# Performance work log

Hardware: AMD Instinct MI355X
Metric: run time of the kernel (lower is better)

Reference implementation:

```python
import jax, jax.numpy as jnp
import numpy as np

BETA = 10.0  # fixed buffer: torch.ones(1, num_centers) * 10


def setup_inputs() -> dict:
    key = jax.random.key(0)
    k1, k2, k3 = jax.random.split(key, 3)
    n, M, d, n_out = 65536, 1024, 64, 3
    x = jax.random.normal(k1, (n, d), dtype=jnp.float32)
    centers = jax.random.normal(k2, (M, d), dtype=jnp.float32)
    # nn.Linear init in the module: weight ~ N(0, 0.02), bias = 0
    W = jax.random.normal(k3, (n_out, M + d), dtype=jnp.float32) * 0.02
    b = jnp.zeros((n_out,), dtype=jnp.float32)
    return {"x": x, "centers": centers, "W": W, "b": b}


def reference(x, centers, W, b):
    x2 = jnp.sum(x * x, axis=1, keepdims=True)          # [n, 1]
    c2 = jnp.sum(centers * centers, axis=1)             # [M]
    d2 = x2 + c2[None, :] - 2.0 * (x @ centers.T)       # [n, M]
    rbf = jnp.exp(-BETA * d2)                           # Gaussian RBF
    feat = jnp.concatenate([x, rbf], axis=1)            # [n, d + M]
    return feat @ W.T + b                               # [n, n_out]
```

## Files before the change

### kernel.cpp

```cpp
#include <hip/hip_runtime.h>
#include <math.h>

typedef short bf16x8 __attribute__((ext_vector_type(8)));
typedef float f32x4 __attribute__((ext_vector_type(4)));
typedef unsigned int uint32;

#define BETA 10.0f
#define THRESH -80.0f

#define C_OFF   0
#define XB_OFF  131072
#define RED_OFF 147456
#define LDS_TOT 150528

__device__ __forceinline__ uint32 f2bf_rtne(float f) {
    uint32 u = __float_as_uint(f);
    u += 0x7FFFu + ((u >> 16) & 1u);
    return u >> 16;
}
__device__ __forceinline__ uint32 pk_rtne(float a, float b) {
    return f2bf_rtne(a) | (f2bf_rtne(b) << 16);
}
__device__ __forceinline__ f32x4 vmax4(f32x4 a, f32x4 b) {
    f32x4 r;
    r[0] = fmaxf(a[0], b[0]); r[1] = fmaxf(a[1], b[1]);
    r[2] = fmaxf(a[2], b[2]); r[3] = fmaxf(a[3], b[3]);
    return r;
}
#define MFMA __builtin_amdgcn_mfma_f32_16x16x32_bf16

__global__ __launch_bounds__(512) void rbfn_fused(
    const float* __restrict__ x,
    const float* __restrict__ centers,
    const float* __restrict__ W,
    const float* __restrict__ bias,
    float* __restrict__ out)
{
    __shared__ __align__(16) char lds[LDS_TOT];

    const int tid = threadIdx.x;
    const int wv = tid >> 6;
    const int lane = tid & 63;
    const int quad = lane >> 4;
    const int l15 = lane & 15;
    const int row0 = blockIdx.x * 256;

    float4 x0[4], x1[4];
    {
        const float4* xg = (const float4*)(x + (size_t)row0 * 64);
        #pragma unroll
        for (int i = 0; i < 4; ++i) x0[i] = xg[i * 512 + tid];
        #pragma unroll
        for (int i = 0; i < 4; ++i) x1[i] = xg[2048 + i * 512 + tid];
    }

    {
        const float4* cf4 = (const float4*)centers;
        #pragma unroll 8
        for (int i = 0; i < 32; ++i) {
            const int f = i * 512 + tid;
            const float4 v = cf4[f];
            const int j = f >> 4, sg = f & 15;
            uint2 q; q.x = pk_rtne(v.x, v.y); q.y = pk_rtne(v.z, v.w);
            *(uint2*)(lds + C_OFF + (j >> 4) * 2048 + (sg >> 1) * 256 +
                      (j & 15) * 16 + (sg & 1) * 8) = q;
        }
    }
    #pragma unroll
    for (int i = 0; i < 4; ++i) {
        const int f = i * 512 + tid;
        const float4 v = x0[i];
        const int r = f >> 4, sg = f & 15;
        uint2 q; q.x = pk_rtne(v.x, v.y); q.y = pk_rtne(v.z, v.w);
        *(uint2*)(lds + XB_OFF + (r >> 4) * 2048 + (sg >> 1) * 256 +
                  (r & 15) * 16 + (sg & 1) * 8) = q;
    }

    bf16x8 bwh[2], bwl[2];
    float bl = 0.f;
    if (wv == 0) {
        if (l15 < 3) bl = bias[l15];
        #pragma unroll
        for (int kk = 0; kk < 2; ++kk) {
            bf16x8 h, l;
            #pragma unroll
            for (int e = 0; e < 8; ++e) {
                const float w = (l15 < 3) ? W[l15 * 1088 + kk * 32 + quad * 8 + e] : 0.f;
                const uint32 hb = f2bf_rtne(w);
                h[e] = (short)hb;
                l[e] = (short)f2bf_rtne(w - __uint_as_float(hb << 16));
            }
            bwh[kk] = h; bwl[kk] = l;
        }
    }

    __syncthreads();

    const char* cB = lds + C_OFF + wv * 16384 + quad * 256 + l15 * 16;
    float c2r[8];

    #pragma unroll
    for (int t = 0; t < 2; ++t) {
        bf16x8 af[8][2];
        #pragma unroll
        for (int rt = 0; rt < 8; ++rt) {
            const char* ab = lds + XB_OFF + rt * 2048 + l15 * 16;
            af[rt][0] = *(const bf16x8*)(ab + quad * 256);
            af[rt][1] = *(const bf16x8*)(ab + (4 + quad) * 256);
        }

        float mn = 1e30f;
        #pragma unroll
        for (int rt = 0; rt < 8; ++rt) {
            const f32x4 z = {0.f, 0.f, 0.f, 0.f};
            f32x4 d = MFMA(af[rt][0], af[rt][0], z, 0, 0, 0);
            d = MFMA(af[rt][1], af[rt][1], d, 0, 0, 0);
            #pragma unroll
            for (int reg = 0; reg < 4; ++reg)
                mn = fminf(mn, __shfl(d[reg], quad * 20 + reg));
        }
        const float prermax = -BETA * mn;

        if (t == 0) {
            #pragma unroll
            for (int ct = 0; ct < 8; ++ct) {
                const bf16x8 b0 = *(const bf16x8*)(cB + ct * 2048);
                const bf16x8 b1 = *(const bf16x8*)(cB + ct * 2048 + 1024);
                const f32x4 z = {0.f, 0.f, 0.f, 0.f};
                f32x4 d = MFMA(b0, b0, z, 0, 0, 0);
                d = MFMA(b1, b1, d, 0, 0, 0);
                const float dv = (l15 & 2) ? ((l15 & 1) ? d[3] : d[2])
                                           : ((l15 & 1) ? d[1] : d[0]);
                c2r[ct] = -BETA * __shfl(dv, (l15 >> 2) * 16 + l15);
            }
        }

        if (wv == 0) {
            float* redf = (float*)(lds + RED_OFF + t * 1536);
            #pragma unroll
            for (int rt = 0; rt < 8; ++rt) {
                const f32x4 z = {0.f, 0.f, 0.f, 0.f};
                f32x4 aw = MFMA(af[rt][0], bwh[0], z, 0, 0, 0);
                aw = MFMA(af[rt][1], bwh[1], aw, 0, 0, 0);
                aw = MFMA(af[rt][0], bwl[0], aw, 0, 0, 0);
                aw = MFMA(af[rt][1], bwl[1], aw, 0, 0, 0);
                if (l15 < 3) {
                    #pragma unroll
                    for (int reg = 0; reg < 4; ++reg)
                        redf[(rt * 16 + quad * 4 + reg) * 3 + l15] = aw[reg] + bl;
                }
            }
        }

        __syncthreads();

        if (t == 0) {
            #pragma unroll
            for (int i = 0; i < 4; ++i) {
                const int f = i * 512 + tid;
                const float4 v = x1[i];
                const int r = f >> 4, sg = f & 15;
                uint2 q; q.x = pk_rtne(v.x, v.y); q.y = pk_rtne(v.z, v.w);
                *(uint2*)(lds + XB_OFF + (r >> 4) * 2048 + (sg >> 1) * 256 +
                          (r & 15) * 16 + (sg & 1) * 8) = q;
            }
        }

        float gm = -1e30f;
        #pragma unroll
        for (int ct = 0; ct < 8; ++ct) {
            const bf16x8 b0 = *(const bf16x8*)(cB + ct * 2048);
            const bf16x8 b1 = *(const bf16x8*)(cB + ct * 2048 + 1024);
            f32x4 acc[8];
            #pragma unroll
            for (int rt = 0; rt < 8; ++rt) {
                const f32x4 z = {0.f, 0.f, 0.f, 0.f};
                acc[rt] = MFMA(af[rt][0], b0, z, 0, 0, 0);
                acc[rt] = MFMA(af[rt][1], b1, acc[rt], 0, 0, 0);
            }
            f32x4 m0 = vmax4(vmax4(acc[0], acc[1]), vmax4(acc[2], acc[3]));
            f32x4 m1 = vmax4(vmax4(acc[4], acc[5]), vmax4(acc[6], acc[7]));
            m0 = vmax4(m0, m1);
            const float m = fmaxf(fmaxf(m0[0], m0[1]), fmaxf(m0[2], m0[3]));
            gm = fmaxf(gm, fmaf(2.0f * BETA, m, c2r[ct]));
        }
        const float bound = gm + prermax;

        if (__builtin_expect(__ballot(bound > THRESH) != 0ull, 0)) {
            float* red = (float*)(lds + RED_OFF + t * 1536);
            #pragma clang loop unroll(disable)
            for (int ct = 0; ct < 8; ++ct) {
                const int j = wv * 128 + ct * 16 + l15;
                #pragma clang loop unroll(disable)
                for (int rr = 0; rr < 32; ++rr) {
                    const int r = (rr >> 2) * 16 + quad * 4 + (rr & 3);
                    const float* xr = x + (size_t)(row0 + t * 128 + r) * 64;
                    const float* cr = centers + (size_t)j * 64;
                    float d2 = 0.f;
                    #pragma clang loop unroll(disable)
                    for (int k = 0; k < 64; ++k) {
                        const float df = xr[k] - cr[k];
                        d2 = fmaf(df, df, d2);
                    }
                    const float arg = -BETA * d2;
                    if (arg > -87.f) {
                        const float e = expf(arg);
                        atomicAdd(&red[r * 3 + 0], e * W[0 * 1088 + 64 + j]);
                        atomicAdd(&red[r * 3 + 1], e * W[1 * 1088 + 64 + j]);
                        atomicAdd(&red[r * 3 + 2], e * W[2 * 1088 + 64 + j]);
                    }
                }
            }
        }
        __syncthreads();

        if (tid < 96)
            ((float4*)out)[blockIdx.x * 192 + t * 96 + tid] =
                *((const float4*)(lds + RED_OFF + t * 1536) + tid);
    }
}

extern "C" void kernel_launch(void* const* d_in, const int* in_sizes, int n_in,
                              void* d_out, int out_size, void* d_ws, size_t ws_size,
                              hipStream_t stream) {
    const float* x       = (const float*)d_in[0];
    const float* centers = (const float*)d_in[1];
    const float* W       = (const float*)d_in[2];
    const float* b       = (const float*)d_in[3];
    float* out = (float*)d_out;

    const int n = in_sizes[0] / 64;
    rbfn_fused<<<n / 256, 512, 0, stream>>>(x, centers, W, b, out);
}
```

Before: 81.51 us.

## Drop LDS staging, load operands into registers, halve rows per block

Result: slower. 99.60 us (+22.2%).

```diff
diff --git a/kernel.cpp b/kernel.cpp
--- a/kernel.cpp
+++ b/kernel.cpp
@@ -7,11 +7,6 @@
 
 #define BETA 10.0f
 #define THRESH -80.0f
-
-#define C_OFF   0
-#define XB_OFF  131072
-#define RED_OFF 147456
-#define LDS_TOT 150528
 
 __device__ __forceinline__ uint32 f2bf_rtne(float f) {
     uint32 u = __float_as_uint(f);
@@ -29,57 +24,81 @@
 }
 #define MFMA __builtin_amdgcn_mfma_f32_16x16x32_bf16
 
-__global__ __launch_bounds__(512) void rbfn_fused(
+__global__ __launch_bounds__(512, 2) void rbfn_fused(
     const float* __restrict__ x,
     const float* __restrict__ centers,
     const float* __restrict__ W,
     const float* __restrict__ bias,
     float* __restrict__ out)
 {
-    __shared__ __align__(16) char lds[LDS_TOT];
+    __shared__ __align__(16) float red[384];
 
     const int tid = threadIdx.x;
     const int wv = tid >> 6;
     const int lane = tid & 63;
     const int quad = lane >> 4;
     const int l15 = lane & 15;
-    const int row0 = blockIdx.x * 256;
+    const int row0 = blockIdx.x * 128;
+    const f32x4 z = {0.f, 0.f, 0.f, 0.f};
 
-    float4 x0[4], x1[4];
-    {
-        const float4* xg = (const float4*)(x + (size_t)row0 * 64);
+    bf16x8 bf[8][2];
+    #pragma unroll
+    for (int ct = 0; ct < 8; ++ct) {
+        const float* cp = centers + (size_t)(wv * 128 + ct * 16 + l15) * 64 + quad * 8;
         #pragma unroll
-        for (int i = 0; i < 4; ++i) x0[i] = xg[i * 512 + tid];
-        #pragma unroll
-        for (int i = 0; i < 4; ++i) x1[i] = xg[2048 + i * 512 + tid];
+        for (int kk = 0; kk < 2; ++kk) {
+            const float4 u0 = *(const float4*)(cp + kk * 32);
+            const float4 u1 = *(const float4*)(cp + kk * 32 + 4);
+            union { bf16x8 v; uint4 u; } t;
+            t.u.x = pk_rtne(u0.x, u0.y);
+            t.u.y = pk_rtne(u0.z, u0.w);
+            t.u.z = pk_rtne(u1.x, u1.y);
+            t.u.w = pk_rtne(u1.z, u1.w);
+            bf[ct][kk] = t.v;
+        }
     }
 
-    {
-        const float4* cf4 = (const float4*)centers;
-        #pragma unroll 8
-        for (int i = 0; i < 32; ++i) {
-            const int f = i * 512 + tid;
-            const float4 v = cf4[f];
-            const int j = f >> 4, sg = f & 15;
-            uint2 q; q.x = pk_rtne(v.x, v.y); q.y = pk_rtne(v.z, v.w);
-            *(uint2*)(lds + C_OFF + (j >> 4) * 2048 + (sg >> 1) * 256 +
-                      (j & 15) * 16 + (sg & 1) * 8) = q;
+    bf16x8 af[8][2];
+    #pragma unroll
+    for (int rt = 0; rt < 8; ++rt) {
+        const float* xp = x + (size_t)(row0 + rt * 16 + l15) * 64 + quad * 8;
+        #pragma unroll
+        for (int kk = 0; kk < 2; ++kk) {
+            const float4 u0 = *(const float4*)(xp + kk * 32);
+            const float4 u1 = *(const float4*)(xp + kk * 32 + 4);
+            union { bf16x8 v; uint4 u; } t;
+            t.u.x = pk_rtne(u0.x, u0.y);
+            t.u.y = pk_rtne(u0.z, u0.w);
+            t.u.z = pk_rtne(u1.x, u1.y);
+            t.u.w = pk_rtne(u1.z, u1.w);
+            af[rt][kk] = t.v;
         }
     }
+
+    float c2r[8];
     #pragma unroll
-    for (int i = 0; i < 4; ++i) {
-        const int f = i * 512 + tid;
-        const float4 v = x0[i];
-        const int r = f >> 4, sg = f & 15;
-        uint2 q; q.x = pk_rtne(v.x, v.y); q.y = pk_rtne(v.z, v.w);
-        *(uint2*)(lds + XB_OFF + (r >> 4) * 2048 + (sg >> 1) * 256 +
-                  (r & 15) * 16 + (sg & 1) * 8) = q;
+    for (int ct = 0; ct < 8; ++ct) {
+        f32x4 d = MFMA(bf[ct][0], bf[ct][0], z, 0, 0, 0);
+        d = MFMA(bf[ct][1], bf[ct][1], d, 0, 0, 0);
+        const float dv = (l15 & 2) ? ((l15 & 1) ? d[3] : d[2])
+                                   : ((l15 & 1) ? d[1] : d[0]);
+        c2r[ct] = -BETA * __shfl(dv, (l15 >> 2) * 16 + l15);
     }
 
-    bf16x8 bwh[2], bwl[2];
-    float bl = 0.f;
+    float mn = 1e30f;
+    #pragma unroll
+    for (int rt = 0; rt < 8; ++rt) {
+        f32x4 d = MFMA(af[rt][0], af[rt][0], z, 0, 0, 0);
+        d = MFMA(af[rt][1], af[rt][1], d, 0, 0, 0);
+        #pragma unroll
+        for (int reg = 0; reg < 4; ++reg)
+            mn = fminf(mn, __shfl(d[reg], quad * 20 + reg));
+    }
+    const float prermax = -BETA * mn;
+
     if (wv == 0) {
-        if (l15 < 3) bl = bias[l15];
+        const float bl = (l15 < 3) ? bias[l15] : 0.f;
+        bf16x8 bwh[2], bwl[2];
         #pragma unroll
         for (int kk = 0; kk < 2; ++kk) {
             bf16x8 h, l;
@@ -92,132 +111,66 @@
             }
             bwh[kk] = h; bwl[kk] = l;
         }
+        #pragma unroll
+        for (int rt = 0; rt < 8; ++rt) {
+            f32x4 aw = MFMA(af[rt][0], bwh[0], z, 0, 0, 0);
+            aw = MFMA(af[rt][1], bwh[1], aw, 0, 0, 0);
+            aw = MFMA(af[rt][0], bwl[0], aw, 0, 0, 0);
+            aw = MFMA(af[rt][1], bwl[1], aw, 0, 0, 0);
+            if (l15 < 3) {
+                #pragma unroll
+                for (int reg = 0; reg < 4; ++reg)
+                    red[(rt * 16 + quad * 4 + reg) * 3 + l15] = aw[reg] + bl;
+            }
+        }
     }
 
-    __syncthreads();
-
-    const char* cB = lds + C_OFF + wv * 16384 + quad * 256 + l15 * 16;
-    float c2r[8];
-
+    float gm = -1e30f;
     #pragma unroll
-    for (int t = 0; t < 2; ++t) {
-        bf16x8 af[8][2];
+    for (int ct = 0; ct < 8; ++ct) {
+        f32x4 acc[8];
         #pragma unroll
         for (int rt = 0; rt < 8; ++rt) {
-            const char* ab = lds + XB_OFF + rt * 2048 + l15 * 16;
-            af[rt][0] = *(const bf16x8*)(ab + quad * 256);
-            af[rt][1] = *(const bf16x8*)(ab + (4 + quad) * 256);
+            acc[rt] = MFMA(af[rt][0], bf[ct][0], z, 0, 0, 0);
+            acc[rt] = MFMA(af[rt][1], bf[ct][1], acc[rt], 0, 0, 0);
         }
+        f32x4 m0 = vmax4(vmax4(acc[0], acc[1]), vmax4(acc[2], acc[3]));
+        f32x4 m1 = vmax4(vmax4(acc[4], acc[5]), vmax4(acc[6], acc[7]));
+        m0 = vmax4(m0, m1);
+        const float m = fmaxf(fmaxf(m0[0], m0[1]), fmaxf(m0[2], m0[3]));
+        gm = fmaxf(gm, fmaf(2.0f * BETA, m, c2r[ct]));
+    }
+    const float bound = gm + prermax;
 
-        float mn = 1e30f;
-        #pragma unroll
-        for (int rt = 0; rt < 8; ++rt) {
-            const f32x4 z = {0.f, 0.f, 0.f, 0.f};
-            f32x4 d = MFMA(af[rt][0], af[rt][0], z, 0, 0, 0);
-            d = MFMA(af[rt][1], af[rt][1], d, 0, 0, 0);
-            #pragma unroll
-            for (int reg = 0; reg < 4; ++reg)
-                mn = fminf(mn, __shfl(d[reg], quad * 20 + reg));
-        }
-        const float prermax = -BETA * mn;
-
-        if (t == 0) {
-            #pragma unroll
-            for (int ct = 0; ct < 8; ++ct) {
-                const bf16x8 b0 = *(const bf16x8*)(cB + ct * 2048);
-                const bf16x8 b1 = *(const bf16x8*)(cB + ct * 2048 + 1024);
-                const f32x4 z = {0.f, 0.f, 0.f, 0.f};
-                f32x4 d = MFMA(b0, b0, z, 0, 0, 0);
-                d = MFMA(b1, b1, d, 0, 0, 0);
-                const float dv = (l15 & 2) ? ((l15 & 1) ? d[3] : d[2])
-                                           : ((l15 & 1) ? d[1] : d[0]);
-                c2r[ct] = -BETA * __shfl(dv, (l15 >> 2) * 16 + l15);
-            }
-        }
-
-        if (wv == 0) {
-            float* redf = (float*)(lds + RED_OFF + t * 1536);
-            #pragma unroll
-            for (int rt = 0; rt < 8; ++rt) {
-                const f32x4 z = {0.f, 0.f, 0.f, 0.f};
-                f32x4 aw = MFMA(af[rt][0], bwh[0], z, 0, 0, 0);
-                aw = MFMA(af[rt][1], bwh[1], aw, 0, 0, 0);
-                aw = MFMA(af[rt][0], bwl[0], aw, 0, 0, 0);
-                aw = MFMA(af[rt][1], bwl[1], aw, 0, 0, 0);
-                if (l15 < 3) {
-                    #pragma unroll
-                    for (int reg = 0; reg < 4; ++reg)
-                        redf[(rt * 16 + quad * 4 + reg) * 3 + l15] = aw[reg] + bl;
+    if (__builtin_expect(__ballot(bound > THRESH) != 0ull, 0)) {
+        #pragma clang loop unroll(disable)
+        for (int ct = 0; ct < 8; ++ct) {
+            const int j = wv * 128 + ct * 16 + l15;
+            #pragma clang loop unroll(disable)
+            for (int rr = 0; rr < 32; ++rr) {
+                const int r = (rr >> 2) * 16 + quad * 4 + (rr & 3);
+                const float* xr = x + (size_t)(row0 + r) * 64;
+                const float* cr = centers + (size_t)j * 64;
+                float d2 = 0.f;
+                #pragma clang loop unroll(disable)
+                for (int k = 0; k < 64; ++k) {
+                    const float df = xr[k] - cr[k];
+                    d2 = fmaf(df, df, d2);
+                }
+                const float arg = -BETA * d2;
+                if (arg > -87.f) {
+                    const float e = expf(arg);
+                    atomicAdd(&red[r * 3 + 0], e * W[0 * 1088 + 64 + j]);
+                    atomicAdd(&red[r * 3 + 1], e * W[1 * 1088 + 64 + j]);
+                    atomicAdd(&red[r * 3 + 2], e * W[2 * 1088 + 64 + j]);
                 }
             }
         }
+    }
+    __syncthreads();
 
-        __syncthreads();
-
-        if (t == 0) {
-            #pragma unroll
-            for (int i = 0; i < 4; ++i) {
-                const int f = i * 512 + tid;
-                const float4 v = x1[i];
-                const int r = f >> 4, sg = f & 15;
-                uint2 q; q.x = pk_rtne(v.x, v.y); q.y = pk_rtne(v.z, v.w);
-                *(uint2*)(lds + XB_OFF + (r >> 4) * 2048 + (sg >> 1) * 256 +
-                          (r & 15) * 16 + (sg & 1) * 8) = q;
-            }
-        }
-
-        float gm = -1e30f;
-        #pragma unroll
-        for (int ct = 0; ct < 8; ++ct) {
-            const bf16x8 b0 = *(const bf16x8*)(cB + ct * 2048);
-            const bf16x8 b1 = *(const bf16x8*)(cB + ct * 2048 + 1024);
-            f32x4 acc[8];
-            #pragma unroll
-            for (int rt = 0; rt < 8; ++rt) {
-                const f32x4 z = {0.f, 0.f, 0.f, 0.f};
-                acc[rt] = MFMA(af[rt][0], b0, z, 0, 0, 0);
-                acc[rt] = MFMA(af[rt][1], b1, acc[rt], 0, 0, 0);
-            }
-            f32x4 m0 = vmax4(vmax4(acc[0], acc[1]), vmax4(acc[2], acc[3]));
-            f32x4 m1 = vmax4(vmax4(acc[4], acc[5]), vmax4(acc[6], acc[7]));
-            m0 = vmax4(m0, m1);
-            const float m = fmaxf(fmaxf(m0[0], m0[1]), fmaxf(m0[2], m0[3]));
-            gm = fmaxf(gm, fmaf(2.0f * BETA, m, c2r[ct]));
-        }
-        const float bound = gm + prermax;
-
-        if (__builtin_expect(__ballot(bound > THRESH) != 0ull, 0)) {
-            float* red = (float*)(lds + RED_OFF + t * 1536);
-            #pragma clang loop unroll(disable)
-            for (int ct = 0; ct < 8; ++ct) {
-                const int j = wv * 128 + ct * 16 + l15;
-                #pragma clang loop unroll(disable)
-                for (int rr = 0; rr < 32; ++rr) {
-                    const int r = (rr >> 2) * 16 + quad * 4 + (rr & 3);
-                    const float* xr = x + (size_t)(row0 + t * 128 + r) * 64;
-                    const float* cr = centers + (size_t)j * 64;
-                    float d2 = 0.f;
-                    #pragma clang loop unroll(disable)
-                    for (int k = 0; k < 64; ++k) {
-                        const float df = xr[k] - cr[k];
-                        d2 = fmaf(df, df, d2);
-                    }
-                    const float arg = -BETA * d2;
-                    if (arg > -87.f) {
-                        const float e = expf(arg);
-                        atomicAdd(&red[r * 3 + 0], e * W[0 * 1088 + 64 + j]);
-                        atomicAdd(&red[r * 3 + 1], e * W[1 * 1088 + 64 + j]);
-                        atomicAdd(&red[r * 3 + 2], e * W[2 * 1088 + 64 + j]);
-                    }
-                }
-            }
-        }
-        __syncthreads();
-
-        if (tid < 96)
-            ((float4*)out)[blockIdx.x * 192 + t * 96 + tid] =
-                *((const float4*)(lds + RED_OFF + t * 1536) + tid);
-    }
+    if (tid < 96)
+        ((float4*)out)[blockIdx.x * 96 + tid] = *((const float4*)red + tid);
 }
 
 extern "C" void kernel_launch(void* const* d_in, const int* in_sizes, int n_in,
@@ -230,5 +183,5 @@
     float* out = (float*)d_out;
 
     const int n = in_sizes[0] / 64;
-    rbfn_fused<<<n / 256, 512, 0, stream>>>(x, centers, W, b, out);
+    rbfn_fused<<<n / 128, 512, 0, stream>>>(x, centers, W, b, out);
 }
```
